# Performance work log

Measured on AMD Instinct MI355X. Metric: run time of the kernel, lower is better.

The kernel has to match this reference:

```python
import jax, jax.numpy as jnp
import numpy as np

M, B, N, C, H = 3, 8, 512, 512, 8
HD = C // H
W_SCALE = 0.02  # keep attention logits in a sane range


def setup_inputs() -> dict:
    key = jax.random.key(0)
    ks = jax.random.split(key, 10)
    f32 = jnp.float32
    return {
        "x": jax.random.normal(ks[0], (M, B, N, C), f32),
        "Wq": jax.random.normal(ks[1], (M, C, C), f32) * W_SCALE,
        "bq": jax.random.normal(ks[2], (M, C), f32) * W_SCALE,
        "Wk": jax.random.normal(ks[3], (M, C, C), f32) * W_SCALE,
        "bk": jax.random.normal(ks[4], (M, C), f32) * W_SCALE,
        "Wv": jax.random.normal(ks[5], (M, C, C), f32) * W_SCALE,
        "bv": jax.random.normal(ks[6], (M, C), f32) * W_SCALE,
        "mw": jnp.ones((M, M), f32),
        "Wp": jax.random.normal(ks[7], (C, C), f32) * W_SCALE,
        "bp": jax.random.normal(ks[8], (C,), f32) * W_SCALE,
    }


def reference(x, Wq, bq, Wk, bk, Wv, bv, mw, Wp, bp):
    # x: [M,B,N,C] stacked modality features
    m, b, n, c = x.shape
    h, hd = H, c // H
    scale = hd ** -0.5

    def project(W, bias):
        y = jnp.einsum('mbnc,mcd->mbnd', x, W) + bias[:, None, None, :]
        return y.reshape(m, b, n, h, hd).transpose(0, 1, 3, 2, 4)  # [M,B,H,N,hd]

    q = project(Wq, bq)
    k = project(Wk, bk)
    v = project(Wv, bv)

    # all M*M pairwise attentions: i = query modality, j = key/value modality
    scores = jnp.einsum('ibhnd,jbhkd->ijbhnk', q, k) * scale  # [M,M,B,H,N,N]
    probs = jax.nn.softmax(scores, axis=-1)
    out = jnp.einsum('ijbhnk,jbhkd->ijbhnd', probs, v)
    out = out * mw[:, :, None, None, None, None]  # per-pair modal weight

    # sum over key-modality j, then mean over query-modality i
    fused = out.sum(axis=1).mean(axis=0)  # [B,H,N,hd]
    fused = fused.transpose(0, 2, 1, 3).reshape(b, n, c)  # [B,N,C]

    return jnp.einsum('bnc,cd->bnd', fused, Wp) + bp
```

## Files before the change

### kernel.cpp

```cpp
#include <hip/hip_runtime.h>
#include <stdint.h>

#define M_ 3
#define B_ 8
#define N_ 512
#define C_ 512
#define H_ 8
#define HD_ 64

typedef __bf16 bf16x8 __attribute__((ext_vector_type(8)));
typedef float f32x4 __attribute__((ext_vector_type(4)));

static __device__ __forceinline__ unsigned short f2bf(float f) {
  unsigned int u = __float_as_uint(f);
  unsigned int r = (u + 0x7FFFu + ((u >> 16) & 1u)) >> 16;
  return (unsigned short)r;
}
static __device__ __forceinline__ float bf2f(unsigned short s) {
  return __uint_as_float(((unsigned int)s) << 16);
}

static __device__ __forceinline__ void gll16(const void* g, void* l) {
  __builtin_amdgcn_global_load_lds(
      (const __attribute__((address_space(1))) unsigned int*)g,
      (__attribute__((address_space(3))) unsigned int*)l, 16, 0, 0);
}

__global__ void convert_x_kernel(const float* __restrict__ x,
                                 unsigned short* __restrict__ xb, int n4) {
  int i = blockIdx.x * 256 + threadIdx.x;
  if (i < n4) {
    float4 v = ((const float4*)x)[i];
    ushort4 o;
    o.x = f2bf(v.x); o.y = f2bf(v.y); o.z = f2bf(v.z); o.w = f2bf(v.w);
    ((ushort4*)xb)[i] = o;
  }
}

__global__ void transpose_w_kernel(const float* __restrict__ Wq, const float* __restrict__ Wk,
                                   const float* __restrict__ Wv, const float* __restrict__ Wp,
                                   unsigned short* __restrict__ Wqt, unsigned short* __restrict__ Wkt,
                                   unsigned short* __restrict__ Wvt, unsigned short* __restrict__ Wpt) {
  int z = blockIdx.z;
  const float* src; unsigned short* dst;
  if (z < 3)      { src = Wq + z * 262144;      dst = Wqt + z * 262144; }
  else if (z < 6) { src = Wk + (z - 3) * 262144; dst = Wkt + (z - 3) * 262144; }
  else if (z < 9) { src = Wv + (z - 6) * 262144; dst = Wvt + (z - 6) * 262144; }
  else            { src = Wp;                    dst = Wpt; }
  __shared__ unsigned short t[64][68];
  int r0 = blockIdx.x * 64, c0 = blockIdx.y * 64;
  int tr = threadIdx.x >> 4, tc = (threadIdx.x & 15) * 4;
#pragma unroll
  for (int it = 0; it < 4; ++it) {
    int r = tr + it * 16;
    float4 v = *(const float4*)&src[(size_t)(r0 + r) * 512 + c0 + tc];
    t[tc + 0][r] = f2bf(v.x); t[tc + 1][r] = f2bf(v.y);
    t[tc + 2][r] = f2bf(v.z); t[tc + 3][r] = f2bf(v.w);
  }
  __syncthreads();
#pragma unroll
  for (int it = 0; it < 4; ++it) {
    int d = tr + it * 16;
    ushort4 o;
    o.x = t[d][tc + 0]; o.y = t[d][tc + 1]; o.z = t[d][tc + 2]; o.w = t[d][tc + 3];
    *(ushort4*)&dst[(size_t)(c0 + d) * 512 + r0 + tc] = o;
  }
}

template <int MODE>
__launch_bounds__(256, 2)
__global__ void gemm128_kernel(const unsigned short* __restrict__ Aall,
                               const unsigned short* __restrict__ Bt0,
                               const unsigned short* __restrict__ Bt1,
                               const unsigned short* __restrict__ Bt2,
                               const float* __restrict__ bias0,
                               const float* __restrict__ bias1,
                               const float* __restrict__ bias2,
                               unsigned short* __restrict__ outQ,
                               unsigned short* __restrict__ outK,
                               unsigned short* __restrict__ outVt,
                               float* __restrict__ outF) {
  const int tid = threadIdx.x;
  const int wv = tid >> 6, l = tid & 63;
  const int wr = wv >> 1, wc = wv & 1;
  const int bm = blockIdx.x, bn = blockIdx.y;
  int m = 0, p = 0;
  const unsigned short* A; const unsigned short* Bt; const float* bias;
  if (MODE == 0) {
    int z = blockIdx.z; m = z / 3; p = z % 3;
    A = Aall + (size_t)m * (B_ * N_ * C_);
    Bt = (p == 0 ? Bt0 : p == 1 ? Bt1 : Bt2) + (size_t)m * (C_ * C_);
    bias = (p == 0 ? bias0 : p == 1 ? bias1 : bias2) + m * C_;
  } else {
    A = Aall; Bt = Bt0; bias = bias0;
  }
  __shared__ __align__(16) unsigned short lA[2][128 * 64];
  __shared__ __align__(16) unsigned short lB[2][128 * 64];
  f32x4 acc[4][4] = {};

  auto stage = [&](int buf, int kt) {
    int k0 = kt * 64;
#pragma unroll
    for (int it = 0; it < 4; ++it) {
      int f = (it * 256 + tid) * 16;
      int r = f >> 7, o = f & 127;
      int so = o ^ ((r & 7) << 4);
      gll16((const char*)A + ((size_t)(bm * 128 + r) * 512 + k0) * 2 + so,
            (char*)&lA[buf][0] + (it * 256 + wv * 64) * 16);
      gll16((const char*)Bt + ((size_t)(bn * 128 + r) * 512 + k0) * 2 + so,
            (char*)&lB[buf][0] + (it * 256 + wv * 64) * 16);
    }
  };

  stage(0, 0);
  __syncthreads();
  int buf = 0;
  for (int kt = 0; kt < 8; ++kt) {
    if (kt < 7) stage(buf ^ 1, kt + 1);
    bf16x8 aF[4][2], bF[4][2];
#pragma unroll
    for (int rt = 0; rt < 4; ++rt)
#pragma unroll
      for (int kf = 0; kf < 2; ++kf) {
        int rowA = wr * 64 + rt * 16 + (l & 15);
        int rowB = wc * 64 + rt * 16 + (l & 15);
        int kb = kf * 64 + (l >> 4) * 16;
        aF[rt][kf] = *(const bf16x8*)((const char*)&lA[buf][0] + rowA * 128 + (kb ^ ((rowA & 7) << 4)));
        bF[rt][kf] = *(const bf16x8*)((const char*)&lB[buf][0] + rowB * 128 + (kb ^ ((rowB & 7) << 4)));
      }
#pragma unroll
    for (int kf = 0; kf < 2; ++kf)
#pragma unroll
      for (int rt = 0; rt < 4; ++rt)
#pragma unroll
        for (int ct = 0; ct < 4; ++ct)
          acc[rt][ct] = __builtin_amdgcn_mfma_f32_16x16x32_bf16(aF[rt][kf], bF[ct][kf], acc[rt][ct], 0, 0, 0);
    __syncthreads();
    buf ^= 1;
  }

#pragma unroll
  for (int rt = 0; rt < 4; ++rt) {
    int rbase = bm * 128 + wr * 64 + rt * 16 + (l >> 4) * 4;
#pragma unroll
    for (int ct = 0; ct < 4; ++ct) {
      int col = bn * 128 + wc * 64 + ct * 16 + (l & 15);
      float bb = bias[col];
      if (MODE == 0) {
        int h = col >> 6, hd = col & 63;
        if (p < 2) {
          unsigned short* out = (p == 0 ? outQ : outK) + (size_t)m * (B_ * H_ * N_ * HD_);
#pragma unroll
          for (int jr = 0; jr < 4; ++jr) {
            int row = rbase + jr; int b = row >> 9, n = row & 511;
            out[(((size_t)(b * H_ + h) * N_ + n) * HD_) + hd] = f2bf(acc[rt][ct][jr] + bb);
          }
        } else {
          unsigned short* out = outVt + (size_t)m * (B_ * H_ * HD_ * N_);
          int row = rbase; int b = row >> 9, n = row & 511;
          ushort4 o;
          o.x = f2bf(acc[rt][ct][0] + bb);
          o.y = f2bf(acc[rt][ct][1] + bb);
          o.z = f2bf(acc[rt][ct][2] + bb);
          o.w = f2bf(acc[rt][ct][3] + bb);
          *(ushort4*)&out[(((size_t)(b * H_ + h) * HD_ + hd) * N_) + n] = o;
        }
      } else {
#pragma unroll
        for (int jr = 0; jr < 4; ++jr) {
          int row = rbase + jr;
          outF[(size_t)row * C_ + col] = acc[rt][ct][jr] + bb;
        }
      }
    }
  }
}

__launch_bounds__(256, 2)
__global__ void attn_kernel(const unsigned short* __restrict__ q,
                            const unsigned short* __restrict__ k,
                            const unsigned short* __restrict__ vt,
                            const float* __restrict__ mw,
                            unsigned short* __restrict__ att) {
  const int tid = threadIdx.x;
  const int wv = tid >> 6, l = tid & 63;
  const int qt = blockIdx.x;
  const int bh = blockIdx.y;
  const int i = blockIdx.z;
  const int b = bh >> 3, h = bh & 7;
  const int n0 = qt * 128;

  __shared__ __align__(16) unsigned short lK[2][64 * 64];
  __shared__ __align__(16) unsigned short lV[2][64 * 64];
  __shared__ __align__(16) unsigned short lP[4][32 * 64];

  bf16x8 aQ[2][2];
  {
    const unsigned short* qb = q + (size_t)((i * B_ + b) * H_ + h) * N_ * HD_;
#pragma unroll
    for (int rt = 0; rt < 2; ++rt)
#pragma unroll
      for (int kf = 0; kf < 2; ++kf) {
        int n = n0 + wv * 32 + rt * 16 + (l & 15);
        aQ[rt][kf] = *(const bf16x8*)&qb[(size_t)n * HD_ + kf * 32 + (l >> 4) * 8];
      }
  }
  bf16x8 ones;
#pragma unroll
  for (int zz = 0; zz < 8; ++zz) ones[zz] = (__bf16)1.0f;

  f32x4 facc[2][4] = {};
  const float scale = 0.125f;

  for (int j = 0; j < 3; ++j) {
    const char* kb = (const char*)(k + (size_t)((j * B_ + b) * H_ + h) * N_ * HD_);
    const char* vb = (const char*)(vt + (size_t)((j * B_ + b) * H_ + h) * HD_ * N_);
    auto stage = [&](int buf, int kt) {
#pragma unroll
      for (int it = 0; it < 2; ++it) {
        int f = (it * 256 + tid) * 16;
        int r = f >> 7, o = f & 127;
        int so = o ^ ((r & 7) << 4);
        gll16(kb + kt * 8192 + (f & ~127) + so, (char*)&lK[buf][0] + (it * 256 + wv * 64) * 16);
        gll16(vb + r * 1024 + kt * 128 + so,    (char*)&lV[buf][0] + (it * 256 + wv * 64) * 16);
      }
    };
    stage(0, 0);
    __syncthreads();
    f32x4 oacc[2][4] = {};
    f32x4 dacc[2] = {};
    int buf = 0;
    for (int kt = 0; kt < 8; ++kt) {
      if (kt < 7) stage(buf ^ 1, kt + 1);
      bf16x8 kB[4][2];
#pragma unroll
      for (int ct = 0; ct < 4; ++ct)
#pragma unroll
        for (int kf = 0; kf < 2; ++kf) {
          int key = ct * 16 + (l & 15);
          int ob = (kf * 64 + (l >> 4) * 16) ^ ((key & 7) << 4);
          kB[ct][kf] = *(const bf16x8*)((const char*)&lK[buf][0] + key * 128 + ob);
        }
      f32x4 s[2][4] = {};
#pragma unroll
      for (int kf = 0; kf < 2; ++kf)
#pragma unroll
        for (int rt = 0; rt < 2; ++rt)
#pragma unroll
          for (int ct = 0; ct < 4; ++ct)
            s[rt][ct] = __builtin_amdgcn_mfma_f32_16x16x32_bf16(aQ[rt][kf], kB[ct][kf], s[rt][ct], 0, 0, 0);
#pragma unroll
      for (int rt = 0; rt < 2; ++rt)
#pragma unroll
        for (int ct = 0; ct < 4; ++ct)
#pragma unroll
          for (int jr = 0; jr < 4; ++jr) {
            int rl = rt * 16 + (l >> 4) * 4 + jr;
            int cb = ((ct * 16 + (l & 15)) * 2) ^ ((rl & 7) << 4);
            float pv = __expf(s[rt][ct][jr] * scale);
            *(unsigned short*)((char*)&lP[wv][0] + rl * 128 + cb) = f2bf(pv);
          }
      asm volatile("s_waitcnt lgkmcnt(0)" ::: "memory");
      bf16x8 pA[2][2];
#pragma unroll
      for (int rt = 0; rt < 2; ++rt)
#pragma unroll
        for (int kf = 0; kf < 2; ++kf) {
          int rl = rt * 16 + (l & 15);
          int ob = (kf * 64 + (l >> 4) * 16) ^ ((rl & 7) << 4);
          pA[rt][kf] = *(const bf16x8*)((const char*)&lP[wv][0] + rl * 128 + ob);
        }
      bf16x8 vB[4][2];
#pragma unroll
      for (int ct = 0; ct < 4; ++ct)
#pragma unroll
        for (int kf = 0; kf < 2; ++kf) {
          int hd = ct * 16 + (l & 15);
          int ob = (kf * 64 + (l >> 4) * 16) ^ ((hd & 7) << 4);
          vB[ct][kf] = *(const bf16x8*)((const char*)&lV[buf][0] + hd * 128 + ob);
        }
#pragma unroll
      for (int kf = 0; kf < 2; ++kf)
#pragma unroll
        for (int rt = 0; rt < 2; ++rt) {
          dacc[rt] = __builtin_amdgcn_mfma_f32_16x16x32_bf16(pA[rt][kf], ones, dacc[rt], 0, 0, 0);
#pragma unroll
          for (int ct = 0; ct < 4; ++ct)
            oacc[rt][ct] = __builtin_amdgcn_mfma_f32_16x16x32_bf16(pA[rt][kf], vB[ct][kf], oacc[rt][ct], 0, 0, 0);
        }
      __syncthreads();
      buf ^= 1;
    }
    float w = mw[i * 3 + j] * (1.0f / 3.0f);
#pragma unroll
    for (int rt = 0; rt < 2; ++rt)
#pragma unroll
      for (int jr = 0; jr < 4; ++jr) {
        float inv = w / dacc[rt][jr];
#pragma unroll
        for (int ct = 0; ct < 4; ++ct)
          facc[rt][ct][jr] += oacc[rt][ct][jr] * inv;
      }
  }
  unsigned short* out = att + (size_t)i * (B_ * N_ * C_);
#pragma unroll
  for (int rt = 0; rt < 2; ++rt)
#pragma unroll
    for (int ct = 0; ct < 4; ++ct) {
      int c = h * 64 + ct * 16 + (l & 15);
#pragma unroll
      for (int jr = 0; jr < 4; ++jr) {
        int n = n0 + wv * 32 + rt * 16 + (l >> 4) * 4 + jr;
        out[((size_t)b * N_ + n) * C_ + c] = f2bf(facc[rt][ct][jr]);
      }
    }
}

__global__ void sum3_kernel(const unsigned short* __restrict__ a0,
                            const unsigned short* __restrict__ a1,
                            const unsigned short* __restrict__ a2,
                            unsigned short* __restrict__ o, int n4) {
  int idx = blockIdx.x * 256 + threadIdx.x;
  if (idx < n4) {
    ushort4 x0 = ((const ushort4*)a0)[idx];
    ushort4 x1 = ((const ushort4*)a1)[idx];
    ushort4 x2 = ((const ushort4*)a2)[idx];
    ushort4 r;
    r.x = f2bf(bf2f(x0.x) + bf2f(x1.x) + bf2f(x2.x));
    r.y = f2bf(bf2f(x0.y) + bf2f(x1.y) + bf2f(x2.y));
    r.z = f2bf(bf2f(x0.z) + bf2f(x1.z) + bf2f(x2.z));
    r.w = f2bf(bf2f(x0.w) + bf2f(x1.w) + bf2f(x2.w));
    ((ushort4*)o)[idx] = r;
  }
}

extern "C" void kernel_launch(void* const* d_in, const int* in_sizes, int n_in,
                              void* d_out, int out_size, void* d_ws, size_t ws_size,
                              hipStream_t stream) {
  const float* x  = (const float*)d_in[0];
  const float* Wq = (const float*)d_in[1];
  const float* bq = (const float*)d_in[2];
  const float* Wk = (const float*)d_in[3];
  const float* bk = (const float*)d_in[4];
  const float* Wv = (const float*)d_in[5];
  const float* bv = (const float*)d_in[6];
  const float* mw = (const float*)d_in[7];
  const float* Wp = (const float*)d_in[8];
  const float* bp = (const float*)d_in[9];
  float* out = (float*)d_out;

  char* ws = (char*)d_ws;
  size_t off = 0;
  auto alloc = [&](size_t elems) {
    unsigned short* pp = (unsigned short*)(ws + off);
    off += elems * 2; off = (off + 255) & ~(size_t)255;
    return pp;
  };
  unsigned short* xb  = alloc((size_t)M_ * B_ * N_ * C_);
  unsigned short* Wqt = alloc((size_t)M_ * C_ * C_);
  unsigned short* Wkt = alloc((size_t)M_ * C_ * C_);
  unsigned short* Wvt = alloc((size_t)M_ * C_ * C_);
  unsigned short* Wpt = alloc((size_t)C_ * C_);
  unsigned short* qb  = alloc((size_t)M_ * B_ * H_ * N_ * HD_);
  unsigned short* kb  = alloc((size_t)M_ * B_ * H_ * N_ * HD_);
  unsigned short* vtb = alloc((size_t)M_ * B_ * H_ * HD_ * N_);
  unsigned short* att = alloc((size_t)M_ * B_ * N_ * C_);
  unsigned short* fb  = alloc((size_t)B_ * N_ * C_);

  convert_x_kernel<<<6144, 256, 0, stream>>>(x, xb, (M_ * B_ * N_ * C_) / 4);
  transpose_w_kernel<<<dim3(8, 8, 10), 256, 0, stream>>>(Wq, Wk, Wv, Wp, Wqt, Wkt, Wvt, Wpt);
  gemm128_kernel<0><<<dim3(32, 4, 9), 256, 0, stream>>>(xb, Wqt, Wkt, Wvt, bq, bk, bv,
                                                        qb, kb, vtb, nullptr);
  attn_kernel<<<dim3(4, 64, 3), 256, 0, stream>>>(qb, kb, vtb, mw, att);
  sum3_kernel<<<2048, 256, 0, stream>>>(att, att + (size_t)B_ * N_ * C_,
                                        att + (size_t)2 * B_ * N_ * C_, fb,
                                        (B_ * N_ * C_) / 4);
  gemm128_kernel<1><<<dim3(32, 4, 1), 256, 0, stream>>>(fb, Wpt, nullptr, nullptr, bp, nullptr, nullptr,
                                                        nullptr, nullptr, nullptr, out);
}
```

Baseline: 218.4 us.

## Rewrite attention with 32x32 MFMA transposed scores and register-resident P

The attention kernel now computes transposed scores (K·Q) with 32x32x16 bf16 MFMAs, so each lane's score outputs can be rearranged with a cross-half lane shuffle into the A-operand layout for the P·V MFMA. This removes the per-wave LDS round trip for P and its wait. The row-sum denominator is now accumulated in scalar registers instead of through a ones-vector MFMA. The grid is flattened and remapped so blocks sharing a (b,h) K/V slice land on the same XCD, and launch bounds raise occupancy to 3 blocks per SM, which adds register pressure.

```diff
diff --git a/kernel.cpp b/kernel.cpp
--- a/kernel.cpp
+++ b/kernel.cpp
@@ -10,6 +10,8 @@
 
 typedef __bf16 bf16x8 __attribute__((ext_vector_type(8)));
 typedef float f32x4 __attribute__((ext_vector_type(4)));
+typedef float f32x16 __attribute__((ext_vector_type(16)));
+typedef unsigned int u32x4 __attribute__((ext_vector_type(4)));
 
 static __device__ __forceinline__ unsigned short f2bf(float f) {
   unsigned int u = __float_as_uint(f);
@@ -176,45 +178,40 @@
   }
 }
 
-__launch_bounds__(256, 2)
-__global__ void attn_kernel(const unsigned short* __restrict__ q,
-                            const unsigned short* __restrict__ k,
-                            const unsigned short* __restrict__ vt,
+__launch_bounds__(256, 3)
+__global__ void attn_kernel(const unsigned short* __restrict__ qg,
+                            const unsigned short* __restrict__ kg,
+                            const unsigned short* __restrict__ vg,
                             const float* __restrict__ mw,
                             unsigned short* __restrict__ att) {
   const int tid = threadIdx.x;
   const int wv = tid >> 6, l = tid & 63;
-  const int qt = blockIdx.x;
-  const int bh = blockIdx.y;
-  const int i = blockIdx.z;
+  const int hi = l >> 5, lq = l & 31;
+  const int xcd = blockIdx.x & 7, slot = blockIdx.x >> 3;
+  const int bh = (xcd << 3) | (slot & 7);
+  const int qi = slot >> 3;
+  const int qt = qi & 3, i = qi >> 2;
   const int b = bh >> 3, h = bh & 7;
   const int n0 = qt * 128;
 
   __shared__ __align__(16) unsigned short lK[2][64 * 64];
   __shared__ __align__(16) unsigned short lV[2][64 * 64];
-  __shared__ __align__(16) unsigned short lP[4][32 * 64];
-
-  bf16x8 aQ[2][2];
+
+  bf16x8 qB[4];
   {
-    const unsigned short* qb = q + (size_t)((i * B_ + b) * H_ + h) * N_ * HD_;
-#pragma unroll
-    for (int rt = 0; rt < 2; ++rt)
-#pragma unroll
-      for (int kf = 0; kf < 2; ++kf) {
-        int n = n0 + wv * 32 + rt * 16 + (l & 15);
-        aQ[rt][kf] = *(const bf16x8*)&qb[(size_t)n * HD_ + kf * 32 + (l >> 4) * 8];
-      }
-  }
-  bf16x8 ones;
-#pragma unroll
-  for (int zz = 0; zz < 8; ++zz) ones[zz] = (__bf16)1.0f;
-
-  f32x4 facc[2][4] = {};
+    const unsigned short* qb = qg + (size_t)((i * B_ + b) * H_ + h) * N_ * HD_;
+    int n = n0 + wv * 32 + lq;
+#pragma unroll
+    for (int ks = 0; ks < 4; ++ks)
+      qB[ks] = *(const bf16x8*)&qb[(size_t)n * HD_ + ks * 16 + hi * 8];
+  }
+
+  f32x16 facc[2] = {};
   const float scale = 0.125f;
 
   for (int j = 0; j < 3; ++j) {
-    const char* kb = (const char*)(k + (size_t)((j * B_ + b) * H_ + h) * N_ * HD_);
-    const char* vb = (const char*)(vt + (size_t)((j * B_ + b) * H_ + h) * HD_ * N_);
+    const char* kb = (const char*)(kg + (size_t)((j * B_ + b) * H_ + h) * N_ * HD_);
+    const char* vb = (const char*)(vg + (size_t)((j * B_ + b) * H_ + h) * HD_ * N_);
     auto stage = [&](int buf, int kt) {
 #pragma unroll
       for (int it = 0; it < 2; ++it) {
@@ -227,92 +224,72 @@
     };
     stage(0, 0);
     __syncthreads();
-    f32x4 oacc[2][4] = {};
-    f32x4 dacc[2] = {};
+    f32x16 oacc[2] = {};
+    float dAcc = 0.0f;
     int buf = 0;
     for (int kt = 0; kt < 8; ++kt) {
       if (kt < 7) stage(buf ^ 1, kt + 1);
-      bf16x8 kB[4][2];
-#pragma unroll
-      for (int ct = 0; ct < 4; ++ct)
-#pragma unroll
-        for (int kf = 0; kf < 2; ++kf) {
-          int key = ct * 16 + (l & 15);
-          int ob = (kf * 64 + (l >> 4) * 16) ^ ((key & 7) << 4);
-          kB[ct][kf] = *(const bf16x8*)((const char*)&lK[buf][0] + key * 128 + ob);
-        }
-      f32x4 s[2][4] = {};
-#pragma unroll
-      for (int kf = 0; kf < 2; ++kf)
-#pragma unroll
-        for (int rt = 0; rt < 2; ++rt)
-#pragma unroll
-          for (int ct = 0; ct < 4; ++ct)
-            s[rt][ct] = __builtin_amdgcn_mfma_f32_16x16x32_bf16(aQ[rt][kf], kB[ct][kf], s[rt][ct], 0, 0, 0);
-#pragma unroll
-      for (int rt = 0; rt < 2; ++rt)
-#pragma unroll
-        for (int ct = 0; ct < 4; ++ct)
-#pragma unroll
-          for (int jr = 0; jr < 4; ++jr) {
-            int rl = rt * 16 + (l >> 4) * 4 + jr;
-            int cb = ((ct * 16 + (l & 15)) * 2) ^ ((rl & 7) << 4);
-            float pv = __expf(s[rt][ct][jr] * scale);
-            *(unsigned short*)((char*)&lP[wv][0] + rl * 128 + cb) = f2bf(pv);
+#pragma unroll
+      for (int kt2 = 0; kt2 < 2; ++kt2) {
+        f32x16 sT = {};
+#pragma unroll
+        for (int ks = 0; ks < 4; ++ks) {
+          int row = kt2 * 32 + lq;
+          int col = (ks * 32 + hi * 16) ^ ((row & 7) << 4);
+          bf16x8 kA = *(const bf16x8*)((const char*)&lK[buf][0] + row * 128 + col);
+          sT = __builtin_amdgcn_mfma_f32_32x32x16_bf16(kA, qB[ks], sT, 0, 0, 0);
+        }
+        unsigned int c[8];
+#pragma unroll
+        for (int w = 0; w < 8; ++w) {
+          float pa = __expf(sT[2 * w] * scale);
+          float pb = __expf(sT[2 * w + 1] * scale);
+          dAcc += pa + pb;
+          c[w] = (unsigned int)f2bf(pa) | ((unsigned int)f2bf(pb) << 16);
+        }
+#pragma unroll
+        for (int hs = 0; hs < 2; ++hs) {
+          int ks = kt2 * 2 + hs;
+          unsigned int p0 = (unsigned int)__shfl_xor((int)c[4 * hs + 0], 32, 64);
+          unsigned int p1 = (unsigned int)__shfl_xor((int)c[4 * hs + 1], 32, 64);
+          unsigned int p2 = (unsigned int)__shfl_xor((int)c[4 * hs + 2], 32, 64);
+          unsigned int p3 = (unsigned int)__shfl_xor((int)c[4 * hs + 3], 32, 64);
+          u32x4 pw;
+          pw.x = hi ? p2 : c[4 * hs + 0];
+          pw.y = hi ? p3 : c[4 * hs + 1];
+          pw.z = hi ? c[4 * hs + 2] : p0;
+          pw.w = hi ? c[4 * hs + 3] : p1;
+          bf16x8 pA = __builtin_bit_cast(bf16x8, pw);
+#pragma unroll
+          for (int ht = 0; ht < 2; ++ht) {
+            int row = ht * 32 + lq;
+            int col = (ks * 32 + hi * 16) ^ ((row & 7) << 4);
+            bf16x8 vB = *(const bf16x8*)((const char*)&lV[buf][0] + row * 128 + col);
+            oacc[ht] = __builtin_amdgcn_mfma_f32_32x32x16_bf16(pA, vB, oacc[ht], 0, 0, 0);
           }
-      asm volatile("s_waitcnt lgkmcnt(0)" ::: "memory");
-      bf16x8 pA[2][2];
-#pragma unroll
-      for (int rt = 0; rt < 2; ++rt)
-#pragma unroll
-        for (int kf = 0; kf < 2; ++kf) {
-          int rl = rt * 16 + (l & 15);
-          int ob = (kf * 64 + (l >> 4) * 16) ^ ((rl & 7) << 4);
-          pA[rt][kf] = *(const bf16x8*)((const char*)&lP[wv][0] + rl * 128 + ob);
-        }
-      bf16x8 vB[4][2];
-#pragma unroll
-      for (int ct = 0; ct < 4; ++ct)
-#pragma unroll
-        for (int kf = 0; kf < 2; ++kf) {
-          int hd = ct * 16 + (l & 15);
-          int ob = (kf * 64 + (l >> 4) * 16) ^ ((hd & 7) << 4);
-          vB[ct][kf] = *(const bf16x8*)((const char*)&lV[buf][0] + hd * 128 + ob);
-        }
-#pragma unroll
-      for (int kf = 0; kf < 2; ++kf)
-#pragma unroll
-        for (int rt = 0; rt < 2; ++rt) {
-          dacc[rt] = __builtin_amdgcn_mfma_f32_16x16x32_bf16(pA[rt][kf], ones, dacc[rt], 0, 0, 0);
-#pragma unroll
-          for (int ct = 0; ct < 4; ++ct)
-            oacc[rt][ct] = __builtin_amdgcn_mfma_f32_16x16x32_bf16(pA[rt][kf], vB[ct][kf], oacc[rt][ct], 0, 0, 0);
-        }
+        }
+      }
       __syncthreads();
       buf ^= 1;
     }
-    float w = mw[i * 3 + j] * (1.0f / 3.0f);
-#pragma unroll
-    for (int rt = 0; rt < 2; ++rt)
-#pragma unroll
-      for (int jr = 0; jr < 4; ++jr) {
-        float inv = w / dacc[rt][jr];
-#pragma unroll
-        for (int ct = 0; ct < 4; ++ct)
-          facc[rt][ct][jr] += oacc[rt][ct][jr] * inv;
-      }
-  }
-  unsigned short* out = att + (size_t)i * (B_ * N_ * C_);
-#pragma unroll
-  for (int rt = 0; rt < 2; ++rt)
-#pragma unroll
-    for (int ct = 0; ct < 4; ++ct) {
-      int c = h * 64 + ct * 16 + (l & 15);
-#pragma unroll
-      for (int jr = 0; jr < 4; ++jr) {
-        int n = n0 + wv * 32 + rt * 16 + (l >> 4) * 4 + jr;
-        out[((size_t)b * N_ + n) * C_ + c] = f2bf(facc[rt][ct][jr]);
-      }
+    float den = dAcc + __shfl_xor(dAcc, 32, 64);
+    float t = mw[i * 3 + j] * (1.0f / 3.0f) / den;
+#pragma unroll
+    for (int reg = 0; reg < 16; ++reg) {
+      int kkq = (reg & 3) + 8 * (reg >> 2) + 4 * hi;
+      float tr = __shfl(t, kkq, 64);
+      facc[0][reg] += oacc[0][reg] * tr;
+      facc[1][reg] += oacc[1][reg] * tr;
+    }
+  }
+  unsigned short* outp = att + (size_t)i * (B_ * N_ * C_);
+#pragma unroll
+  for (int ht = 0; ht < 2; ++ht)
+#pragma unroll
+    for (int reg = 0; reg < 16; ++reg) {
+      int n = n0 + wv * 32 + (reg & 3) + 8 * (reg >> 2) + 4 * hi;
+      int cc = h * 64 + ht * 32 + lq;
+      outp[((size_t)b * N_ + n) * C_ + cc] = f2bf(facc[ht][reg]);
     }
 }
 
@@ -371,7 +348,7 @@
   transpose_w_kernel<<<dim3(8, 8, 10), 256, 0, stream>>>(Wq, Wk, Wv, Wp, Wqt, Wkt, Wvt, Wpt);
   gemm128_kernel<0><<<dim3(32, 4, 9), 256, 0, stream>>>(xb, Wqt, Wkt, Wvt, bq, bk, bv,
                                                         qb, kb, vtb, nullptr);
-  attn_kernel<<<dim3(4, 64, 3), 256, 0, stream>>>(qb, kb, vtb, mw, att);
+  attn_kernel<<<768, 256, 0, stream>>>(qb, kb, vtb, mw, att);
   sum3_kernel<<<2048, 256, 0, stream>>>(att, att + (size_t)B_ * N_ * C_,
                                         att + (size_t)2 * B_ * N_ * C_, fb,
                                         (B_ * N_ * C_) / 4);
```

Result: no change. 214.5 us (-1.8%).
